# Kernel tuning notes

Hardware: AMD Instinct MI355X
Metric: run time of the kernel (lower is better)

The kernel has to match this reference:

```python
import jax, jax.numpy as jnp
import numpy as np

E = 768
H = 12
D = E // H
HID = 3072
NEXP = 4
TOPK = 2
EPS = 1e-5


def _ln(x, g, b):
    m = jnp.mean(x, axis=-1, keepdims=True)
    v = jnp.mean(jnp.square(x - m), axis=-1, keepdims=True)
    return (x - m) * jax.lax.rsqrt(v + EPS) * g + b


def setup_inputs() -> dict:
    key = jax.random.key(0)
    ks = jax.random.split(key, 10)
    s = 0.02  # xavier-ish scale so activations stay sane
    return {
        "x": jax.random.normal(ks[0], (8, 1024, E), jnp.float32),
        "ln1_g": jnp.ones((E,), jnp.float32),
        "ln1_b": jnp.zeros((E,), jnp.float32),
        "in_w": jax.random.normal(ks[1], (3 * E, E), jnp.float32) * s,
        "in_b": jnp.zeros((3 * E,), jnp.float32),
        "out_w": jax.random.normal(ks[2], (E, E), jnp.float32) * s,
        "out_b": jnp.zeros((E,), jnp.float32),
        "mlp_w1": jax.random.normal(ks[3], (E, HID), jnp.float32) * s,
        "mlp_b1": jnp.zeros((HID,), jnp.float32),
        "mlp_w2": jax.random.normal(ks[4], (HID, E), jnp.float32) * s,
        "mlp_b2": jnp.zeros((E,), jnp.float32),
        "ln2_g": jnp.ones((E,), jnp.float32),
        "ln2_b": jnp.zeros((E,), jnp.float32),
        "gate_w": jax.random.normal(ks[5], (NEXP, E), jnp.float32) * s,
        "gate_b": jnp.zeros((NEXP,), jnp.float32),
        "exp_w1": jax.random.normal(ks[6], (NEXP, E, HID), jnp.float32) * s,
        "exp_b1": jnp.zeros((NEXP, HID), jnp.float32),
        "exp_w2": jax.random.normal(ks[7], (NEXP, HID, E), jnp.float32) * s,
        "exp_b2": jnp.zeros((NEXP, E), jnp.float32),
    }


def reference(x, ln1_g, ln1_b, in_w, in_b, out_w, out_b,
              mlp_w1, mlp_b1, mlp_w2, mlp_b2,
              ln2_g, ln2_b, gate_w, gate_b,
              exp_w1, exp_b1, exp_w2, exp_b2):
    B, N, _ = x.shape
    # ---- self-attention (torch MultiheadAttention, batch_first) ----
    h = _ln(x, ln1_g, ln1_b)
    qkv = h @ in_w.T + in_b                      # [B,N,3E]
    q, k, v = jnp.split(qkv, 3, axis=-1)
    q = q.reshape(B, N, H, D)
    k = k.reshape(B, N, H, D)
    v = v.reshape(B, N, H, D)
    scores = jnp.einsum('bqhd,bkhd->bhqk', q, k) / jnp.sqrt(jnp.float32(D))
    attn = jax.nn.softmax(scores, axis=-1)
    ctx = jnp.einsum('bhqk,bkhd->bqhd', attn, v).reshape(B, N, E)
    x = x + ctx @ out_w.T + out_b                # dropout = identity (eval)
    # ---- MLP (note: no pre-norm in the original) ----
    x = x + jax.nn.gelu(x @ mlp_w1 + mlp_b1, approximate=False) @ mlp_w2 + mlp_b2
    # ---- MoE ----
    xm = _ln(x, ln2_g, ln2_b)
    logits = xm @ gate_w.T + gate_b              # [B,N,NEXP]
    topv, topi = jax.lax.top_k(logits, TOPK)     # [B,N,k]
    gates = jax.nn.softmax(topv, axis=-1)
    onehot = jax.nn.one_hot(topi, NEXP, dtype=x.dtype)       # [B,N,k,NEXP]
    comb = jnp.einsum('bnk,bnke->bne', gates, onehot)        # per-expert weight
    moe_out = jnp.zeros_like(x)
    for e in range(NEXP):  # small fixed expert count
        he = jax.nn.gelu(xm @ exp_w1[e] + exp_b1[e], approximate=False)
        oe = he @ exp_w2[e] + exp_b2[e]
        moe_out = moe_out + comb[..., e:e + 1] * oe
    return x + moe_out
```

## Files before the change

kernel.cpp:

```cpp
#include <hip/hip_runtime.h>


typedef _Float16 f16;
typedef _Float16 f16x4 __attribute__((ext_vector_type(4)));
typedef _Float16 f16x8 __attribute__((ext_vector_type(8)));
typedef float f32x4 __attribute__((ext_vector_type(4)));
typedef unsigned short ushort;

#define MFMA16(a, b, c) __builtin_amdgcn_mfma_f32_16x16x32_f16((a), (b), (c), 0, 0, 0)

__device__ __forceinline__ void gload16(void* lds, const void* g) {
  __builtin_amdgcn_global_load_lds(
      (const __attribute__((address_space(1))) unsigned int*)g,
      (__attribute__((address_space(3))) unsigned int*)lds, 16, 0, 0);
}

__device__ __forceinline__ void split2(float t, f16& h, f16& l) {
  h = (f16)t;
  l = (f16)(t - (float)h);
}

__device__ __forceinline__ float gelu_f(float x) {
  return 0.5f * x * (1.0f + erff(x * 0.70710678118654752f));
}

__device__ __forceinline__ float gelu_fast(float x) {
  return x / (1.0f + __expf(-1.5957691216f * (x + 0.044715f * x * x * x)));
}

__global__ __launch_bounds__(256) void ln_kernel(
    const float* __restrict__ x, const float* __restrict__ gam,
    const float* __restrict__ bet, f16* __restrict__ oh, f16* __restrict__ ol) {
  const int w = threadIdx.x >> 6, lane = threadIdx.x & 63;
  const size_t row = (size_t)blockIdx.x * 4 + w;
  const float* xr = x + row * 768;
  f32x4 v[3];
  float s = 0.0f;
#pragma unroll
  for (int c = 0; c < 3; c++) {
    v[c] = *(const f32x4*)(xr + c * 256 + lane * 4);
    s += v[c][0] + v[c][1] + v[c][2] + v[c][3];
  }
#pragma unroll
  for (int off = 32; off; off >>= 1) s += __shfl_xor(s, off);
  const float mean = s * (1.0f / 768.0f);
  float q = 0.0f;
#pragma unroll
  for (int c = 0; c < 3; c++)
#pragma unroll
    for (int j = 0; j < 4; j++) {
      float d = v[c][j] - mean;
      q += d * d;
    }
#pragma unroll
  for (int off = 32; off; off >>= 1) q += __shfl_xor(q, off);
  const float rstd = 1.0f / sqrtf(q * (1.0f / 768.0f) + 1e-5f);
#pragma unroll
  for (int c = 0; c < 3; c++) {
    const int col = c * 256 + lane * 4;
    f32x4 gv = *(const f32x4*)(gam + col);
    f32x4 bv = *(const f32x4*)(bet + col);
    f16x4 yh, yl;
#pragma unroll
    for (int j = 0; j < 4; j++) {
      float y = (v[c][j] - mean) * rstd * gv[j] + bv[j];
      f16 hh, ll;
      split2(y, hh, ll);
      yh[j] = hh;
      yl[j] = ll;
    }
    *(f16x4*)(oh + row * 768 + col) = yh;
    *(f16x4*)(ol + row * 768 + col) = yl;
  }
}

__global__ __launch_bounds__(256) void convert_split_k(
    const float* __restrict__ in, f16* __restrict__ oh, f16* __restrict__ ol,
    int n4) {
  const int i = blockIdx.x * 256 + threadIdx.x;
  if (i >= n4) return;
  f32x4 v = ((const f32x4*)in)[i];
  f16x4 h, l;
#pragma unroll
  for (int j = 0; j < 4; j++) {
    f16 hh, ll;
    split2(v[j], hh, ll);
    h[j] = hh;
    l[j] = ll;
  }
  ((f16x4*)oh)[i] = h;
  ((f16x4*)ol)[i] = l;
}

__global__ __launch_bounds__(256) void transpose_k(
    const float* __restrict__ in, f16* __restrict__ oh, f16* __restrict__ ol,
    int R, int ldin) {
  __shared__ float t[32][33];
  const int tx = threadIdx.x & 31, ty = threadIdx.x >> 5;
  const int r0 = blockIdx.y * 32, c0 = blockIdx.x * 32;
#pragma unroll
  for (int i = 0; i < 4; i++)
    t[ty + 8 * i][tx] = in[(size_t)(r0 + ty + 8 * i) * ldin + c0 + tx];
  __syncthreads();
#pragma unroll
  for (int i = 0; i < 4; i++) {
    const float val = t[tx][ty + 8 * i];
    const size_t o = (size_t)(c0 + ty + 8 * i) * R + r0 + tx;
    f16 hh, ll;
    split2(val, hh, ll);
    oh[o] = hh;
    ol[o] = ll;
  }
}

__global__ __launch_bounds__(256) void etrans_kernel(
    const float* __restrict__ in0, f16* __restrict__ out0, int R, int C) {
  const size_t eoff = (size_t)blockIdx.z * R * C;
  const float* in = in0 + eoff;
  f16* out = out0 + eoff;
  __shared__ float t[32][33];
  const int tx = threadIdx.x & 31, ty = threadIdx.x >> 5;
  const int r0 = blockIdx.y * 32, c0 = blockIdx.x * 32;
#pragma unroll
  for (int i = 0; i < 4; i++)
    t[ty + 8 * i][tx] = in[(size_t)(r0 + ty + 8 * i) * C + c0 + tx];
  __syncthreads();
#pragma unroll
  for (int i = 0; i < 4; i++)
    out[(size_t)(c0 + ty + 8 * i) * R + r0 + tx] = (f16)t[tx][ty + 8 * i];
}

__global__ __launch_bounds__(256) void vtrans_kernel(
    const ushort* __restrict__ srcH, const ushort* __restrict__ srcL,
    ushort* __restrict__ dstH, ushort* __restrict__ dstL) {
  const int nt = blockIdx.x, bh = blockIdx.y;
  const ushort* src = blockIdx.z ? srcL : srcH;
  ushort* dst = blockIdx.z ? dstL : dstH;
  const int b = bh / 12, h = bh % 12;
  __shared__ ushort t[64][65];
  const int tid = threadIdx.x;
#pragma unroll
  for (int i = 0; i < 16; i++) {
    const int idx = i * 256 + tid;
    const int r = idx >> 6, c = idx & 63;
    t[r][c] = src[((size_t)b * 1024 + nt * 64 + r) * 2304 + 1536 + h * 64 + c];
  }
  __syncthreads();
#pragma unroll
  for (int i = 0; i < 16; i++) {
    const int idx = i * 256 + tid;
    const int d = idx >> 6, n = idx & 63;
    dst[((size_t)bh * 64 + d) * 1024 + nt * 64 + n] = t[n][d];
  }
}

template <int MODE>
__global__ __launch_bounds__(256) void gemm_split(
    const f16* __restrict__ Ah, const f16* __restrict__ Al, int lda,
    const f16* __restrict__ Bh, const f16* __restrict__ Bl, int ldb,
    const float* __restrict__ bias, const float* __restrict__ residF,
    const f16* __restrict__ residH, const f16* __restrict__ residL, int addto,
    float* __restrict__ outF, f16* __restrict__ outH, f16* __restrict__ outL,
    int ldo, int K, int nbx) {
  __shared__ __align__(16) f16 Ash[128][64];
  __shared__ __align__(16) f16 Asl[128][64];
  __shared__ __align__(16) f16 Bsh[128][64];
  __shared__ __align__(16) f16 Bsl[128][64];
  const int per = gridDim.x >> 3;
  const int lin = ((int)blockIdx.x & 7) * per + ((int)blockIdx.x >> 3);
  const int bx = lin % nbx, by = lin / nbx;
  const int tid = threadIdx.x;
  const int lane = tid & 63, wid = tid >> 6;
  const int wm = wid >> 1, wn = wid & 1;
  const int g = lane >> 4, lr = lane & 15;
  const int swz = (((tid & 7) ^ ((tid >> 3) & 7)) << 3);
  const size_t m0 = (size_t)by * 128, n0 = (size_t)bx * 128;
  f32x4 acc[4][4] = {};
  for (int k0 = 0; k0 < K; k0 += 64) {
    __syncthreads();
#pragma unroll
    for (int s = 0; s < 4; s++) {
      const int u = s * 256 + tid;
      const int row = u >> 3;
      const size_t ga = (m0 + row) * (size_t)lda + k0 + swz;
      const size_t gb = (n0 + row) * (size_t)ldb + k0 + swz;
      gload16(&Ash[0][0] + u * 8, Ah + ga);
      gload16(&Asl[0][0] + u * 8, Al + ga);
      gload16(&Bsh[0][0] + u * 8, Bh + gb);
      gload16(&Bsl[0][0] + u * 8, Bl + gb);
    }
    __syncthreads();
#pragma unroll
    for (int kk = 0; kk < 2; kk++) {
      f16x8 fah[4], fal[4], fbh[4], fbl[4];
#pragma unroll
      for (int mi = 0; mi < 4; mi++) {
        const int row = wm * 64 + mi * 16 + lr;
        const int c = (((kk * 4 + g) ^ (lr & 7)) << 3);
        fah[mi] = *(const f16x8*)&Ash[row][c];
        fal[mi] = *(const f16x8*)&Asl[row][c];
      }
#pragma unroll
      for (int ni = 0; ni < 4; ni++) {
        const int row = wn * 64 + ni * 16 + lr;
        const int c = (((kk * 4 + g) ^ (lr & 7)) << 3);
        fbh[ni] = *(const f16x8*)&Bsh[row][c];
        fbl[ni] = *(const f16x8*)&Bsl[row][c];
      }
#pragma unroll
      for (int mi = 0; mi < 4; mi++)
#pragma unroll
        for (int ni = 0; ni < 4; ni++) {
          acc[mi][ni] = MFMA16(fah[mi], fbh[ni], acc[mi][ni]);
          acc[mi][ni] = MFMA16(fah[mi], fbl[ni], acc[mi][ni]);
          acc[mi][ni] = MFMA16(fal[mi], fbh[ni], acc[mi][ni]);
        }
    }
  }
#pragma unroll
  for (int ni = 0; ni < 4; ni++) {
    const size_t col = n0 + wn * 64 + ni * 16 + lr;
    const float bv = bias ? bias[col] : 0.0f;
#pragma unroll
    for (int mi = 0; mi < 4; mi++) {
      const size_t rowb = m0 + wm * 64 + mi * 16 + g * 4;
      const f32x4 c = acc[mi][ni];
#pragma unroll
      for (int r = 0; r < 4; r++) {
        const size_t idx = (rowb + r) * (size_t)ldo + col;
        const float v = c[r] + bv;
        if constexpr (MODE == 0) {
          f16 hh, ll;
          split2(v, hh, ll);
          outH[idx] = hh;
          outL[idx] = ll;
        } else if constexpr (MODE == 1) {
          const float tt = v + residF[idx];
          f16 hh, ll;
          split2(tt, hh, ll);
          outH[idx] = hh;
          outL[idx] = ll;
        } else if constexpr (MODE == 2) {
          const float tt = gelu_f(v);
          f16 hh, ll;
          split2(tt, hh, ll);
          outH[idx] = hh;
          outL[idx] = ll;
        } else {
          outF[idx] = addto ? (outF[idx] + v)
                            : ((float)residH[idx] + (float)residL[idx] + v);
        }
      }
    }
  }
}

__global__ __launch_bounds__(256) void gemm_moe1(
    const f16* __restrict__ xmh, const f16* __restrict__ etw1,
    const float* __restrict__ eb1, const int* __restrict__ lists,
    const int* __restrict__ cnts, const int* __restrict__ starts,
    f16* __restrict__ ehid, int hf) {
  const int per = gridDim.x >> 3;
  const int lin = (blockIdx.x & 7) * per + (blockIdx.x >> 3);
  const int bx = lin % 12, by = lin / 12;
  const int m0 = by * 128;
  if (m0 >= starts[4]) return;
  int e = 0;
  while (e < 3 && m0 >= starts[e + 1]) e++;
  const int cnt = cnts[e];
  const int loc0 = m0 - starts[e];
  const int* list = lists + e * 8192;
  const f16* Bw = etw1 + ((size_t)e * 3072 + hf * 1536) * 768;
  const float* bias = eb1 + e * 3072 + hf * 1536;
  __shared__ __align__(16) f16 As0[128][64], Bs0[128][64];
  __shared__ __align__(16) f16 As1[128][64], Bs1[128][64];
  const int tid = threadIdx.x;
  const int lane = tid & 63, wid = tid >> 6;
  const int wm = wid >> 1, wn = wid & 1;
  const int g = lane >> 4, lr = lane & 15;
  const int swz = (((tid & 7) ^ ((tid >> 3) & 7)) << 3);
  const int n0 = bx * 128;
  size_t arow[4];
#pragma unroll
  for (int s = 0; s < 4; s++) {
    const int row = (s * 256 + tid) >> 3;
    const int loc = loc0 + row;
    arow[s] = (size_t)list[loc < cnt ? loc : cnt - 1] * 768;
  }
  f32x4 acc[4][4] = {};
  auto STAGE = [&](f16 (&A)[128][64], f16 (&B)[128][64], int k0) {
#pragma unroll
    for (int s = 0; s < 4; s++) {
      const int u = s * 256 + tid;
      const int row = u >> 3;
      gload16(&A[0][0] + u * 8, xmh + arow[s] + k0 + swz);
      gload16(&B[0][0] + u * 8, Bw + (size_t)(n0 + row) * 768 + k0 + swz);
    }
  };
  auto COMPUTE = [&](f16 (&A)[128][64], f16 (&B)[128][64]) {
#pragma unroll
    for (int kk = 0; kk < 2; kk++) {
      f16x8 fa[4], fb[4];
#pragma unroll
      for (int mi = 0; mi < 4; mi++) {
        const int row = wm * 64 + mi * 16 + lr;
        fa[mi] = *(const f16x8*)&A[row][(((kk * 4 + g) ^ (lr & 7)) << 3)];
      }
#pragma unroll
      for (int ni = 0; ni < 4; ni++) {
        const int row = wn * 64 + ni * 16 + lr;
        fb[ni] = *(const f16x8*)&B[row][(((kk * 4 + g) ^ (lr & 7)) << 3)];
      }
#pragma unroll
      for (int mi = 0; mi < 4; mi++)
#pragma unroll
        for (int ni = 0; ni < 4; ni++)
          acc[mi][ni] = MFMA16(fa[mi], fb[ni], acc[mi][ni]);
    }
  };
  STAGE(As0, Bs0, 0);
#pragma unroll
  for (int t = 0; t < 12; t += 2) {
    __syncthreads();
    if (t + 1 < 12) STAGE(As1, Bs1, (t + 1) * 64);
    COMPUTE(As0, Bs0);
    __syncthreads();
    if (t + 2 < 12) STAGE(As0, Bs0, (t + 2) * 64);
    COMPUTE(As1, Bs1);
  }
#pragma unroll
  for (int ni = 0; ni < 4; ni++) {
    const int col = n0 + wn * 64 + ni * 16 + lr;
    const float bv = bias[col];
#pragma unroll
    for (int mi = 0; mi < 4; mi++) {
      const int gr = m0 + wm * 64 + mi * 16 + g * 4;
      const f32x4 c = acc[mi][ni];
#pragma unroll
      for (int r = 0; r < 4; r++)
        ehid[(size_t)(gr + r) * 1536 + col] = (f16)gelu_fast(c[r] + bv);
    }
  }
}

__global__ __launch_bounds__(256) void gemm_moe2(
    const f16* __restrict__ ehid, const f16* __restrict__ etw2,
    const float* __restrict__ eb2, const float* __restrict__ comb,
    const int* __restrict__ lists, const int* __restrict__ cnts,
    const int* __restrict__ starts, f16* __restrict__ eout, int hf) {
  const int per = gridDim.x >> 3;
  const int lin = (blockIdx.x & 7) * per + (blockIdx.x >> 3);
  const int bx = lin % 6, by = lin / 6;
  const int m0 = by * 128;
  if (m0 >= starts[4]) return;
  int e = 0;
  while (e < 3 && m0 >= starts[e + 1]) e++;
  const int cnt = cnts[e];
  const int st = starts[e];
  const int* list = lists + e * 8192;
  const f16* Bw = etw2 + (size_t)e * 768 * 3072 + hf * 1536;
  __shared__ __align__(16) f16 As0[128][64], Bs0[128][64];
  __shared__ __align__(16) f16 As1[128][64], Bs1[128][64];
  const int tid = threadIdx.x;
  const int lane = tid & 63, wid = tid >> 6;
  const int wm = wid >> 1, wn = wid & 1;
  const int g = lane >> 4, lr = lane & 15;
  const int swz = (((tid & 7) ^ ((tid >> 3) & 7)) << 3);
  const int n0 = bx * 128;
  f32x4 acc[4][4] = {};
  auto STAGE = [&](f16 (&A)[128][64], f16 (&B)[128][64], int k0) {
#pragma unroll
    for (int s = 0; s < 4; s++) {
      const int u = s * 256 + tid;
      const int row = u >> 3;
      gload16(&A[0][0] + u * 8, ehid + (size_t)(m0 + row) * 1536 + k0 + swz);
      gload16(&B[0][0] + u * 8, Bw + (size_t)(n0 + row) * 3072 + k0 + swz);
    }
  };
  auto COMPUTE = [&](f16 (&A)[128][64], f16 (&B)[128][64]) {
#pragma unroll
    for (int kk = 0; kk < 2; kk++) {
      f16x8 fa[4], fb[4];
#pragma unroll
      for (int mi = 0; mi < 4; mi++) {
        const int row = wm * 64 + mi * 16 + lr;
        fa[mi] = *(const f16x8*)&A[row][(((kk * 4 + g) ^ (lr & 7)) << 3)];
      }
#pragma unroll
      for (int ni = 0; ni < 4; ni++) {
        const int row = wn * 64 + ni * 16 + lr;
        fb[ni] = *(const f16x8*)&B[row][(((kk * 4 + g) ^ (lr & 7)) << 3)];
      }
#pragma unroll
      for (int mi = 0; mi < 4; mi++)
#pragma unroll
        for (int ni = 0; ni < 4; ni++)
          acc[mi][ni] = MFMA16(fa[mi], fb[ni], acc[mi][ni]);
    }
  };
  STAGE(As0, Bs0, 0);
#pragma unroll
  for (int t = 0; t < 24; t += 2) {
    __syncthreads();
    if (t + 1 < 24) STAGE(As1, Bs1, (t + 1) * 64);
    COMPUTE(As0, Bs0);
    __syncthreads();
    if (t + 2 < 24) STAGE(As0, Bs0, (t + 2) * 64);
    COMPUTE(As1, Bs1);
  }
#pragma unroll
  for (int ni = 0; ni < 4; ni++) {
    const int col = n0 + wn * 64 + ni * 16 + lr;
    const float bv = hf ? 0.0f : eb2[e * 768 + col];
#pragma unroll
    for (int mi = 0; mi < 4; mi++) {
      const int gr = m0 + wm * 64 + mi * 16 + g * 4;
      const f32x4 c = acc[mi][ni];
#pragma unroll
      for (int r = 0; r < 4; r++) {
        const int loc = gr + r - st;
        if (loc < cnt) {
          const int tok = list[loc];
          const float w = comb[(size_t)tok * 4 + e];
          const size_t oi = (size_t)(gr + r) * 768 + col;
          const float v = w * (c[r] + bv);
          eout[oi] = hf ? (f16)((float)eout[oi] + v) : (f16)v;
        }
      }
    }
  }
}

__global__ __launch_bounds__(256) void combine_kernel(
    float* __restrict__ out, const f16* __restrict__ eout,
    const int* __restrict__ posA, const int* __restrict__ posB) {
  const int w = threadIdx.x >> 6, lane = threadIdx.x & 63;
  const size_t row = (size_t)blockIdx.x * 4 + w;
  const size_t pa = (size_t)posA[row] * 768, pb = (size_t)posB[row] * 768;
#pragma unroll
  for (int c = 0; c < 3; c++) {
    const int col = c * 256 + lane * 4;
    f32x4 v = *(const f32x4*)(out + row * 768 + col);
    const f16x4 a = *(const f16x4*)(eout + pa + col);
    const f16x4 b = *(const f16x4*)(eout + pb + col);
#pragma unroll
    for (int j = 0; j < 4; j++) v[j] += (float)a[j] + (float)b[j];
    *(f32x4*)(out + row * 768 + col) = v;
  }
}

__global__ __launch_bounds__(256) void attn_kernel(
    const f16* __restrict__ qh, const f16* __restrict__ ql,
    const f16* __restrict__ vth, const f16* __restrict__ vtl,
    f16* __restrict__ ch, f16* __restrict__ cl) {
  const int wg = blockIdx.y * 16 + blockIdx.x;
  const int nid = (wg & 7) * 192 + (wg >> 3);
  const int qt = nid & 15, bh = nid >> 4;
  const int b = bh / 12, h = bh % 12;
  const int tid = threadIdx.x;
  const int lane = tid & 63, w = tid >> 6;
  const int g = lane >> 4, lr = lane & 15;
  __shared__ __align__(16) f16 Ksh[64][64];
  __shared__ __align__(16) f16 Ksl[64][64];
  __shared__ __align__(16) f16 Vsh[64][64];
  __shared__ __align__(16) f16 Vsl[64][64];
  __shared__ __align__(16) char Psh[4][2048];
  const int swz = (((tid & 7) ^ ((tid >> 3) & 7)) << 3);
  const size_t qrow = (size_t)b * 1024 + qt * 64 + w * 16 + lr;
  const f16* qbh = qh + qrow * 2304 + h * 64;
  const f16x8 qfh0 = *(const f16x8*)(qbh + g * 8);
  const f16x8 qfh1 = *(const f16x8*)(qbh + 32 + g * 8);
  const f16x8 ones = {(f16)1, (f16)1, (f16)1, (f16)1, (f16)1, (f16)1, (f16)1, (f16)1};
  f32x4 o[4] = {};
  f32x4 osum = {};
  const f16* kbh = qh + ((size_t)b * 1024) * 2304 + 768 + h * 64;
  const f16* kbl = ql + ((size_t)b * 1024) * 2304 + 768 + h * 64;
  const f16* vbh = vth + (size_t)bh * 64 * 1024;
  const f16* vbl = vtl + (size_t)bh * 64 * 1024;
  char* pbh = Psh[w];
  for (int kv0 = 0; kv0 < 1024; kv0 += 64) {
    __syncthreads();
#pragma unroll
    for (int s = 0; s < 2; s++) {
      const int u = s * 256 + tid;
      const int row = u >> 3;
      const size_t ko = (size_t)(kv0 + row) * 2304 + swz;
      gload16(&Ksh[0][0] + u * 8, kbh + ko);
      gload16(&Ksl[0][0] + u * 8, kbl + ko);
      const size_t vo = (size_t)row * 1024 + kv0 + swz;
      gload16(&Vsh[0][0] + u * 8, vbh + vo);
      gload16(&Vsl[0][0] + u * 8, vbl + vo);
    }
    __syncthreads();
    f32x4 s[4];
    __builtin_amdgcn_s_setprio(1);
#pragma unroll
    for (int nb = 0; nb < 4; nb++) {
      const int row = nb * 16 + lr;
      const int c0 = ((g ^ (lr & 7)) << 3);
      const int c1 = (((4 + g) ^ (lr & 7)) << 3);
      const f16x8 kh0 = *(const f16x8*)&Ksh[row][c0];
      const f16x8 kh1 = *(const f16x8*)&Ksh[row][c1];
      const f16x8 kl0 = *(const f16x8*)&Ksl[row][c0];
      const f16x8 kl1 = *(const f16x8*)&Ksl[row][c1];
      f32x4 t = {};
      t = MFMA16(qfh0, kh0, t);
      t = MFMA16(qfh1, kh1, t);
      t = MFMA16(qfh0, kl0, t);
      t = MFMA16(qfh1, kl1, t);
      s[nb] = t;
    }
    __builtin_amdgcn_s_setprio(0);
#pragma unroll
    for (int nb = 0; nb < 4; nb++)
#pragma unroll
      for (int r = 0; r < 4; r++) {
        const int row = g * 4 + r;
        const int sw = ((nb * 16 + lr) * 2) ^ ((row & 7) << 4);
        *(f16*)(pbh + row * 128 + sw) = (f16)__expf(s[nb][r] * 0.125f);
      }
    __builtin_amdgcn_s_setprio(1);
#pragma unroll
    for (int ks = 0; ks < 2; ks++) {
      const int pc = (ks * 64 + g * 16) ^ ((lr & 7) << 4);
      const f16x8 pfh = *(const f16x8*)(pbh + lr * 128 + pc);
      osum = MFMA16(pfh, ones, osum);
#pragma unroll
      for (int db = 0; db < 4; db++) {
        const int vrow = db * 16 + lr;
        const int vc = (((ks * 4 + g) ^ (lr & 7)) << 3);
        const f16x8 vfh = *(const f16x8*)&Vsh[vrow][vc];
        const f16x8 vfl = *(const f16x8*)&Vsl[vrow][vc];
        o[db] = MFMA16(pfh, vfh, o[db]);
        o[db] = MFMA16(pfh, vfl, o[db]);
      }
    }
    __builtin_amdgcn_s_setprio(0);
  }
  const size_t orow = (size_t)b * 1024 + qt * 64 + w * 16 + g * 4;
#pragma unroll
  for (int r = 0; r < 4; r++) {
    const float inv = 1.0f / osum[r];
#pragma unroll
    for (int db = 0; db < 4; db++) {
      const float val = o[db][r] * inv;
      const size_t oi = (orow + r) * 768 + h * 64 + db * 16 + lr;
      f16 hh, ll;
      split2(val, hh, ll);
      ch[oi] = hh;
      cl[oi] = ll;
    }
  }
}

__global__ __launch_bounds__(256) void gate_kernel(
    const f16* __restrict__ xmh, const f16* __restrict__ xml,
    const float* __restrict__ gw, const float* __restrict__ gb,
    float* __restrict__ comb) {
  const int t = blockIdx.x * 256 + threadIdx.x;
  const f16* xrh = xmh + (size_t)t * 768;
  const f16* xrl = xml + (size_t)t * 768;
  float a0 = 0, a1 = 0, a2 = 0, a3 = 0;
  for (int k = 0; k < 768; k += 4) {
    const f16x4 xh = *(const f16x4*)(xrh + k);
    const f16x4 xl = *(const f16x4*)(xrl + k);
    const f32x4 w0 = *(const f32x4*)(gw + k);
    const f32x4 w1 = *(const f32x4*)(gw + 768 + k);
    const f32x4 w2 = *(const f32x4*)(gw + 1536 + k);
    const f32x4 w3 = *(const f32x4*)(gw + 2304 + k);
#pragma unroll
    for (int j = 0; j < 4; j++) {
      const float xv = (float)xh[j] + (float)xl[j];
      a0 += xv * w0[j];
      a1 += xv * w1[j];
      a2 += xv * w2[j];
      a3 += xv * w3[j];
    }
  }
  float l[4] = {a0 + gb[0], a1 + gb[1], a2 + gb[2], a3 + gb[3]};
  int i0 = 0;
#pragma unroll
  for (int e = 1; e < 4; e++)
    if (l[e] > l[i0]) i0 = e;
  int i1 = -1;
#pragma unroll
  for (int e = 0; e < 4; e++)
    if (e != i0 && (i1 < 0 || l[e] > l[i1])) i1 = e;
  const float e1 = expf(l[i1] - l[i0]);
  const float inv = 1.0f / (1.0f + e1);
  float c[4] = {0.0f, 0.0f, 0.0f, 0.0f};
  c[i0] = inv;
  c[i1] = e1 * inv;
  f32x4 cv = {c[0], c[1], c[2], c[3]};
  *(f32x4*)(comb + (size_t)t * 4) = cv;
}

__global__ __launch_bounds__(1024) void listbuild_kernel(
    const float* __restrict__ comb, int* __restrict__ lists ,
    int* __restrict__ cnts , int* __restrict__ starts ,
    int* __restrict__ posA , int* __restrict__ posB ) {
  __shared__ int wsum[16];
  const int tid = threadIdx.x;
  const int lane = tid & 63, wv = tid >> 6;
  unsigned seen = 0;
  int segbase = 0;
  for (int e = 0; e < 4; e++) {
    int base = 0;
    for (int c = 0; c < 8; c++) {
      const int t = c * 1024 + tid;
      const int flag = comb[(size_t)t * 4 + e] > 0.0f ? 1 : 0;
      const unsigned long long mask = __ballot(flag);
      const int myrank = __popcll(mask & ((1ull << lane) - 1ull));
      if (lane == 0) wsum[wv] = __popcll(mask);
      __syncthreads();
      int wbase = 0, total = 0;
#pragma unroll
      for (int i = 0; i < 16; i++) {
        if (i < wv) wbase += wsum[i];
        total += wsum[i];
      }
      if (flag) {
        const int idx = base + wbase + myrank;
        lists[e * 8192 + idx] = t;
        const int gidx = segbase + idx;
        if ((seen >> c) & 1) posB[t] = gidx;
        else { posA[t] = gidx; seen |= 1u << c; }
      }
      base += total;
      __syncthreads();
    }
    if (tid == 0) cnts[e] = base;
    segbase += (base + 127) & ~127;
  }
  if (tid == 0) {
    int s = 0;
    starts[0] = 0;
#pragma unroll
    for (int e = 0; e < 4; e++) {
      s += (cnts[e] + 127) & ~127;
      starts[e + 1] = s;
    }
  }
}

extern "C" void kernel_launch(void* const* d_in, const int* in_sizes, int n_in,
                              void* d_out, int out_size, void* d_ws,
                              size_t ws_size, hipStream_t stream) {
  const float* x = (const float*)d_in[0];
  const float* ln1g = (const float*)d_in[1];
  const float* ln1b = (const float*)d_in[2];
  const float* in_w = (const float*)d_in[3];
  const float* in_b = (const float*)d_in[4];
  const float* out_w = (const float*)d_in[5];
  const float* out_b = (const float*)d_in[6];
  const float* mlp_w1 = (const float*)d_in[7];
  const float* mlp_b1 = (const float*)d_in[8];
  const float* mlp_w2 = (const float*)d_in[9];
  const float* mlp_b2 = (const float*)d_in[10];
  const float* ln2g = (const float*)d_in[11];
  const float* ln2b = (const float*)d_in[12];
  const float* gate_w = (const float*)d_in[13];
  const float* gate_b = (const float*)d_in[14];
  const float* exp_w1 = (const float*)d_in[15];
  const float* exp_b1 = (const float*)d_in[16];
  const float* exp_w2 = (const float*)d_in[17];
  const float* exp_b2 = (const float*)d_in[18];
  float* out = (float*)d_out;
  (void)in_sizes; (void)n_in; (void)out_size;

  const size_t MB = 1ull << 20;
  if (ws_size < 130 * MB) return;
  char* ws = (char*)d_ws;
  char* S1 = ws;
  char* S2 = ws + 24 * MB;
  char* S3 = ws + 33 * MB;
  char* S4 = ws + 105 * MB;
  char* S5 = ws + 129 * MB;

  f16* h_h = (f16*)S1;
  f16* h_l = (f16*)(S1 + 12 * MB);
  f16* ctx_h = (f16*)S1;
  f16* ctx_l = (f16*)(S1 + 12 * MB);
  f16* w1t_h = (f16*)S1;
  f16* w1t_l = (f16*)(S1 + 4718592);
  f16* xmh = (f16*)S1;
  f16* xml = (f16*)(S1 + 12 * MB);

  f16* inw_h = (f16*)S2;
  f16* inw_l = (f16*)(S2 + 3538944);
  f16* outw_h = (f16*)(S2 + 7077888);
  f16* outw_l = (f16*)(S2 + 8257536);
  f16* w2t_h = (f16*)S2;
  f16* w2t_l = (f16*)(S2 + 4718592);

  f16* qkv_h = (f16*)S3;
  f16* qkv_l = (f16*)(S3 + 36 * MB);
  f16* hid_h = (f16*)S3;
  f16* hid_l = (f16*)(S3 + 24 * MB);

  f16* vt_h = (f16*)S4;
  f16* vt_l = (f16*)(S4 + 12 * MB);
  f16* x1h = (f16*)S4;
  f16* x1l = (f16*)(S4 + 12 * MB);

  f16* etw1 = (f16*)(ws + 12 * MB);
  f16* etw2 = (f16*)(ws + 30 * MB);
  f16* ehid = (f16*)(ws + 48 * MB);
  f16* eout = (f16*)(ws + 100 * MB);

  float* comb = (float*)S5;
  int* lists = (int*)(S5 + 131072);
  int* cnts = (int*)(S5 + 262144);
  int* starts = (int*)(S5 + 262144 + 64);
  int* posA = (int*)(S5 + 262144 + 256);
  int* posB = (int*)(S5 + 262144 + 256 + 32768);

  convert_split_k<<<dim3(1728), dim3(256), 0, stream>>>(in_w, inw_h, inw_l, 442368);
  convert_split_k<<<dim3(576), dim3(256), 0, stream>>>(out_w, outw_h, outw_l, 147456);
  ln_kernel<<<dim3(2048), dim3(256), 0, stream>>>(x, ln1g, ln1b, h_h, h_l);
  gemm_split<0><<<dim3(1152), dim3(256), 0, stream>>>(
      h_h, h_l, 768, inw_h, inw_l, 768, in_b, nullptr, nullptr, nullptr, 0,
      nullptr, qkv_h, qkv_l, 2304, 768, 18);
  vtrans_kernel<<<dim3(16, 96, 2), dim3(256), 0, stream>>>(
      (const ushort*)qkv_h, (const ushort*)qkv_l, (ushort*)vt_h, (ushort*)vt_l);
  attn_kernel<<<dim3(16, 96), dim3(256), 0, stream>>>(qkv_h, qkv_l, vt_h, vt_l, ctx_h, ctx_l);
  gemm_split<1><<<dim3(384), dim3(256), 0, stream>>>(
      ctx_h, ctx_l, 768, outw_h, outw_l, 768, out_b, x, nullptr, nullptr, 0,
      nullptr, x1h, x1l, 768, 768, 6);

  transpose_k<<<dim3(96, 24), dim3(256), 0, stream>>>(mlp_w1, w1t_h, w1t_l, 768, 3072);
  transpose_k<<<dim3(24, 96), dim3(256), 0, stream>>>(mlp_w2, w2t_h, w2t_l, 3072, 768);
  gemm_split<2><<<dim3(768), dim3(256), 0, stream>>>(
      x1h, x1l, 768, w1t_h, w1t_l, 768, mlp_b1, nullptr, nullptr, nullptr, 0,
      nullptr, hid_h, hid_l, 1536, 768, 12);
  gemm_split<3><<<dim3(384), dim3(256), 0, stream>>>(
      hid_h, hid_l, 1536, w2t_h, w2t_l, 3072, mlp_b2, nullptr, x1h, x1l, 0,
      out, nullptr, nullptr, 768, 1536, 6);
  gemm_split<2><<<dim3(768), dim3(256), 0, stream>>>(
      x1h, x1l, 768, w1t_h + (size_t)1536 * 768, w1t_l + (size_t)1536 * 768, 768,
      mlp_b1 + 1536, nullptr, nullptr, nullptr, 0, nullptr, hid_h, hid_l, 1536, 768, 12);
  gemm_split<3><<<dim3(384), dim3(256), 0, stream>>>(
      hid_h, hid_l, 1536, w2t_h + 1536, w2t_l + 1536, 3072,
      nullptr, nullptr, nullptr, nullptr, 1, out, nullptr, nullptr, 768, 1536, 6);

  ln_kernel<<<dim3(2048), dim3(256), 0, stream>>>(out, ln2g, ln2b, xmh, xml);
  gate_kernel<<<dim3(32), dim3(256), 0, stream>>>(xmh, xml, gate_w, gate_b, comb);
  listbuild_kernel<<<dim3(1), dim3(1024), 0, stream>>>(comb, lists, cnts, starts, posA, posB);
  etrans_kernel<<<dim3(96, 24, 4), dim3(256), 0, stream>>>(exp_w1, etw1, 768, 3072);
  etrans_kernel<<<dim3(24, 96, 4), dim3(256), 0, stream>>>(exp_w2, etw2, 3072, 768);
  for (int hf = 0; hf < 2; hf++) {
    gemm_moe1<<<dim3(1584), dim3(256), 0, stream>>>(
        xmh, etw1, exp_b1, lists, cnts, starts, ehid, hf);
    gemm_moe2<<<dim3(792), dim3(256), 0, stream>>>(
        ehid, etw2, exp_b2, comb, lists, cnts, starts, eout, hf);
  }
  combine_kernel<<<dim3(2048), dim3(256), 0, stream>>>(out, eout, posA, posB);
}
```

Baseline: 1.002 ms.

## Shrink MoE GEMM tiles to 64 rows and drop LDS double buffering

Both expert GEMM kernels now use 64x128 tiles with four waves split along N, and the grid size is doubled to match. The two-stage LDS double buffer is replaced by a single buffer loaded synchronously each k-step. The aim is more blocks and higher occupancy from smaller LDS use. In exchange, each wave does fewer MFMAs per load and global-load latency is no longer overlapped with compute.

```diff
diff --git a/kernel.cpp b/kernel.cpp
--- a/kernel.cpp
+++ b/kernel.cpp
@@ -263,7 +263,7 @@
   const int per = gridDim.x >> 3;
   const int lin = (blockIdx.x & 7) * per + (blockIdx.x >> 3);
   const int bx = lin % 12, by = lin / 12;
-  const int m0 = by * 128;
+  const int m0 = by * 64;
   if (m0 >= starts[4]) return;
   int e = 0;
   while (e < 3 && m0 >= starts[e + 1]) e++;
@@ -272,69 +272,58 @@
   const int* list = lists + e * 8192;
   const f16* Bw = etw1 + ((size_t)e * 3072 + hf * 1536) * 768;
   const float* bias = eb1 + e * 3072 + hf * 1536;
-  __shared__ __align__(16) f16 As0[128][64], Bs0[128][64];
-  __shared__ __align__(16) f16 As1[128][64], Bs1[128][64];
+  __shared__ __align__(16) f16 As[64][64];
+  __shared__ __align__(16) f16 Bs[128][64];
   const int tid = threadIdx.x;
-  const int lane = tid & 63, wid = tid >> 6;
-  const int wm = wid >> 1, wn = wid & 1;
+  const int lane = tid & 63, wn = tid >> 6;
   const int g = lane >> 4, lr = lane & 15;
   const int swz = (((tid & 7) ^ ((tid >> 3) & 7)) << 3);
   const int n0 = bx * 128;
-  size_t arow[4];
-#pragma unroll
-  for (int s = 0; s < 4; s++) {
+  size_t arow[2];
+#pragma unroll
+  for (int s = 0; s < 2; s++) {
     const int row = (s * 256 + tid) >> 3;
     const int loc = loc0 + row;
     arow[s] = (size_t)list[loc < cnt ? loc : cnt - 1] * 768;
   }
-  f32x4 acc[4][4] = {};
-  auto STAGE = [&](f16 (&A)[128][64], f16 (&B)[128][64], int k0) {
+  f32x4 acc[4][2] = {};
+  for (int k0 = 0; k0 < 768; k0 += 64) {
+    __syncthreads();
+#pragma unroll
+    for (int s = 0; s < 2; s++) {
+      const int u = s * 256 + tid;
+      gload16(&As[0][0] + u * 8, xmh + arow[s] + k0 + swz);
+    }
 #pragma unroll
     for (int s = 0; s < 4; s++) {
       const int u = s * 256 + tid;
       const int row = u >> 3;
-      gload16(&A[0][0] + u * 8, xmh + arow[s] + k0 + swz);
-      gload16(&B[0][0] + u * 8, Bw + (size_t)(n0 + row) * 768 + k0 + swz);
-    }
-  };
-  auto COMPUTE = [&](f16 (&A)[128][64], f16 (&B)[128][64]) {
+      gload16(&Bs[0][0] + u * 8, Bw + (size_t)(n0 + row) * 768 + k0 + swz);
+    }
+    __syncthreads();
 #pragma unroll
     for (int kk = 0; kk < 2; kk++) {
-      f16x8 fa[4], fb[4];
-#pragma unroll
-      for (int mi = 0; mi < 4; mi++) {
-        const int row = wm * 64 + mi * 16 + lr;
-        fa[mi] = *(const f16x8*)&A[row][(((kk * 4 + g) ^ (lr & 7)) << 3)];
-      }
-#pragma unroll
-      for (int ni = 0; ni < 4; ni++) {
-        const int row = wn * 64 + ni * 16 + lr;
-        fb[ni] = *(const f16x8*)&B[row][(((kk * 4 + g) ^ (lr & 7)) << 3)];
-      }
+      const int c = (((kk * 4 + g) ^ (lr & 7)) << 3);
+      f16x8 fa[4], fb[2];
+#pragma unroll
+      for (int mi = 0; mi < 4; mi++) fa[mi] = *(const f16x8*)&As[mi * 16 + lr][c];
+#pragma unroll
+      for (int ni = 0; ni < 2; ni++)
+        fb[ni] = *(const f16x8*)&Bs[wn * 32 + ni * 16 + lr][c];
 #pragma unroll
       for (int mi = 0; mi < 4; mi++)
 #pragma unroll
-        for (int ni = 0; ni < 4; ni++)
+        for (int ni = 0; ni < 2; ni++)
           acc[mi][ni] = MFMA16(fa[mi], fb[ni], acc[mi][ni]);
     }
-  };
-  STAGE(As0, Bs0, 0);
-#pragma unroll
-  for (int t = 0; t < 12; t += 2) {
-    __syncthreads();
-    if (t + 1 < 12) STAGE(As1, Bs1, (t + 1) * 64);
-    COMPUTE(As0, Bs0);
-    __syncthreads();
-    if (t + 2 < 12) STAGE(As0, Bs0, (t + 2) * 64);
-    COMPUTE(As1, Bs1);
-  }
-#pragma unroll
-  for (int ni = 0; ni < 4; ni++) {
-    const int col = n0 + wn * 64 + ni * 16 + lr;
+  }
+#pragma unroll
+  for (int ni = 0; ni < 2; ni++) {
+    const int col = n0 + wn * 32 + ni * 16 + lr;
     const float bv = bias[col];
 #pragma unroll
     for (int mi = 0; mi < 4; mi++) {
-      const int gr = m0 + wm * 64 + mi * 16 + g * 4;
+      const int gr = m0 + mi * 16 + g * 4;
       const f32x4 c = acc[mi][ni];
 #pragma unroll
       for (int r = 0; r < 4; r++)
@@ -351,7 +340,7 @@
   const int per = gridDim.x >> 3;
   const int lin = (blockIdx.x & 7) * per + (blockIdx.x >> 3);
   const int bx = lin % 6, by = lin / 6;
-  const int m0 = by * 128;
+  const int m0 = by * 64;
   if (m0 >= starts[4]) return;
   int e = 0;
   while (e < 3 && m0 >= starts[e + 1]) e++;
@@ -359,62 +348,52 @@
   const int st = starts[e];
   const int* list = lists + e * 8192;
   const f16* Bw = etw2 + (size_t)e * 768 * 3072 + hf * 1536;
-  __shared__ __align__(16) f16 As0[128][64], Bs0[128][64];
-  __shared__ __align__(16) f16 As1[128][64], Bs1[128][64];
+  __shared__ __align__(16) f16 As[64][64];
+  __shared__ __align__(16) f16 Bs[128][64];
   const int tid = threadIdx.x;
-  const int lane = tid & 63, wid = tid >> 6;
-  const int wm = wid >> 1, wn = wid & 1;
+  const int lane = tid & 63, wn = tid >> 6;
   const int g = lane >> 4, lr = lane & 15;
   const int swz = (((tid & 7) ^ ((tid >> 3) & 7)) << 3);
   const int n0 = bx * 128;
-  f32x4 acc[4][4] = {};
-  auto STAGE = [&](f16 (&A)[128][64], f16 (&B)[128][64], int k0) {
+  f32x4 acc[4][2] = {};
+  for (int k0 = 0; k0 < 1536; k0 += 64) {
+    __syncthreads();
+#pragma unroll
+    for (int s = 0; s < 2; s++) {
+      const int u = s * 256 + tid;
+      const int row = u >> 3;
+      gload16(&As[0][0] + u * 8, ehid + (size_t)(m0 + row) * 1536 + k0 + swz);
+    }
 #pragma unroll
     for (int s = 0; s < 4; s++) {
       const int u = s * 256 + tid;
       const int row = u >> 3;
-      gload16(&A[0][0] + u * 8, ehid + (size_t)(m0 + row) * 1536 + k0 + swz);
-      gload16(&B[0][0] + u * 8, Bw + (size_t)(n0 + row) * 3072 + k0 + swz);
-    }
-  };
-  auto COMPUTE = [&](f16 (&A)[128][64], f16 (&B)[128][64]) {
+      gload16(&Bs[0][0] + u * 8, Bw + (size_t)(n0 + row) * 3072 + k0 + swz);
+    }
+    __syncthreads();
 #pragma unroll
     for (int kk = 0; kk < 2; kk++) {
-      f16x8 fa[4], fb[4];
-#pragma unroll
-      for (int mi = 0; mi < 4; mi++) {
-        const int row = wm * 64 + mi * 16 + lr;
-        fa[mi] = *(const f16x8*)&A[row][(((kk * 4 + g) ^ (lr & 7)) << 3)];
-      }
-#pragma unroll
-      for (int ni = 0; ni < 4; ni++) {
-        const int row = wn * 64 + ni * 16 + lr;
-        fb[ni] = *(const f16x8*)&B[row][(((kk * 4 + g) ^ (lr & 7)) << 3)];
-      }
+      const int c = (((kk * 4 + g) ^ (lr & 7)) << 3);
+      f16x8 fa[4], fb[2];
+#pragma unroll
+      for (int mi = 0; mi < 4; mi++) fa[mi] = *(const f16x8*)&As[mi * 16 + lr][c];
+#pragma unroll
+      for (int ni = 0; ni < 2; ni++)
+        fb[ni] = *(const f16x8*)&Bs[wn * 32 + ni * 16 + lr][c];
 #pragma unroll
       for (int mi = 0; mi < 4; mi++)
 #pragma unroll
-        for (int ni = 0; ni < 4; ni++)
+        for (int ni = 0; ni < 2; ni++)
           acc[mi][ni] = MFMA16(fa[mi], fb[ni], acc[mi][ni]);
     }
-  };
-  STAGE(As0, Bs0, 0);
-#pragma unroll
-  for (int t = 0; t < 24; t += 2) {
-    __syncthreads();
-    if (t + 1 < 24) STAGE(As1, Bs1, (t + 1) * 64);
-    COMPUTE(As0, Bs0);
-    __syncthreads();
-    if (t + 2 < 24) STAGE(As0, Bs0, (t + 2) * 64);
-    COMPUTE(As1, Bs1);
-  }
-#pragma unroll
-  for (int ni = 0; ni < 4; ni++) {
-    const int col = n0 + wn * 64 + ni * 16 + lr;
+  }
+#pragma unroll
+  for (int ni = 0; ni < 2; ni++) {
+    const int col = n0 + wn * 32 + ni * 16 + lr;
     const float bv = hf ? 0.0f : eb2[e * 768 + col];
 #pragma unroll
     for (int mi = 0; mi < 4; mi++) {
-      const int gr = m0 + wm * 64 + mi * 16 + g * 4;
+      const int gr = m0 + mi * 16 + g * 4;
       const f32x4 c = acc[mi][ni];
 #pragma unroll
       for (int r = 0; r < 4; r++) {
@@ -749,9 +728,9 @@
   etrans_kernel<<<dim3(96, 24, 4), dim3(256), 0, stream>>>(exp_w1, etw1, 768, 3072);
   etrans_kernel<<<dim3(24, 96, 4), dim3(256), 0, stream>>>(exp_w2, etw2, 3072, 768);
   for (int hf = 0; hf < 2; hf++) {
-    gemm_moe1<<<dim3(1584), dim3(256), 0, stream>>>(
+    gemm_moe1<<<dim3(3168), dim3(256), 0, stream>>>(
         xmh, etw1, exp_b1, lists, cnts, starts, ehid, hf);
-    gemm_moe2<<<dim3(792), dim3(256), 0, stream>>>(
+    gemm_moe2<<<dim3(1584), dim3(256), 0, stream>>>(
         ehid, etw2, exp_b2, comb, lists, cnts, starts, eout, hf);
   }
   combine_kernel<<<dim3(2048), dim3(256), 0, stream>>>(out, eout, posA, posB);
```

Result: faster. 937.2 us (-6.5%).
